# Kernel optimization log

Measured on AMD Instinct MI355X. Metric: run time of the kernel, lower is better.

The kernel has to match this reference:

```python
import jax, jax.numpy as jnp
import numpy as np

T, N, D, R, E = 512, 32, 300, 3, 64
NUM_NODES, VG = 70000, 40000


def setup_inputs() -> dict:
    key = jax.random.key(0)
    ks = jax.random.split(key, 10)
    return {
        "x_indices": jax.random.randint(ks[0], (T, N), 0, NUM_NODES),
        "edge_src": jax.random.randint(ks[1], (T, R, E), 0, N),
        "edge_dst": jax.random.randint(ks[2], (T, R, E), 0, N),
        "X": jax.random.normal(ks[3], (NUM_NODES, D), dtype=jnp.float32) * 0.1,
        "conv_W": jax.random.normal(ks[4], (R, D, D), dtype=jnp.float32) * 0.05,
        "W0": jax.random.normal(ks[5], (D, D), dtype=jnp.float32) * 0.05,
        "Wu": jax.random.normal(ks[6], (N * D, D), dtype=jnp.float32) * 0.01,
        "Uu": jax.random.normal(ks[7], (D, D), dtype=jnp.float32) * 0.05,
        "Wg": jax.random.normal(ks[8], (VG, D), dtype=jnp.float32) * 0.05,
        "bg": jnp.zeros((VG,), dtype=jnp.float32),
    }


def gcn_conv(x, W, src, dst):
    """torch_geometric GCNConv(bias=False): add self-loops, D^-1/2 (A+I) D^-1/2 (x W)."""
    n = x.shape[0]
    h = x @ W  # [N, D]
    loop = jnp.arange(n)
    s = jnp.concatenate([src, loop])
    t = jnp.concatenate([dst, loop])
    deg = jax.ops.segment_sum(jnp.ones_like(t, dtype=x.dtype), t, num_segments=n)
    dinv = jnp.where(deg > 0, jax.lax.rsqrt(jnp.maximum(deg, 1e-12)), 0.0)
    norm = dinv[s] * dinv[t]  # [E+N]
    return jax.ops.segment_sum(h[s] * norm[:, None], t, num_segments=n)


def reference(x_indices, edge_src, edge_dst, X, conv_W, W0, Wu, Uu, Wg, bg):
    def step(mem, inp):
        idx, src, dst = inp  # [N], [R,E], [R,E]
        x = X[idx]  # grapharea features [N, D]
        # sum of per-relation GCNConv outputs
        conv = jnp.sum(
            jax.vmap(gcn_conv, in_axes=(None, 0, 0, 0))(x, conv_W, src, dst), axis=0
        )
        proposed = conv + x @ W0  # eye(N) @ (x @ W0) == x @ W0
        # GRU-style update gate: [1, N*D] @ [N*D, D] + mem_row0 @ [D, D]
        gate = jax.nn.sigmoid(x.reshape(1, -1) @ Wu + mem[0:1] @ Uu)  # [1, D]
        new_mem = gate * proposed + (1.0 - gate) * mem  # broadcast over N rows
        logits = jnp.maximum(new_mem[0], 0.0) @ Wg.T + bg  # [VG]
        # memory is a non-grad buffer in torch (.data.copy_): stop gradient through time
        return jax.lax.stop_gradient(new_mem), jax.nn.log_softmax(logits)

    mem0 = jnp.zeros((N, D), dtype=X.dtype)
    _, log_probs = jax.lax.scan(step, mem0, (x_indices, edge_src, edge_dst))
    # include_senses=False: per-step torch.tensor(0) stacked -> zeros([T])
    return log_probs, jnp.zeros((x_indices.shape[0],), dtype=jnp.int32)
```

## Files before the change

### kernel.cpp

```cpp
#include <hip/hip_runtime.h>
#include <hip/hip_bf16.h>
#include <math.h>

#define T_ 512
#define N_ 32
#define D_ 300
#define R_ 3
#define E_ 64
#define VG_ 40000

typedef __attribute__((ext_vector_type(8))) short bf16x8;
typedef __attribute__((ext_vector_type(4))) float f32x4;

#define LGKM_BARRIER() asm volatile("s_waitcnt lgkmcnt(0)\n\ts_barrier" ::: "memory")

static __device__ inline unsigned short f2b(float f) {
  __hip_bfloat16 h = __float2bfloat16(f);
  return *(unsigned short*)&h;
}

__global__ void k_zero(float* __restrict__ p, int n) {
  int i = blockIdx.x * blockDim.x + threadIdx.x;
  if (i < n) p[i] = 0.f;
}

__global__ void k_tr_wu(const float* __restrict__ Wu, unsigned short* __restrict__ Wt) {
  __shared__ float s[32][33];
  int kb = blockIdx.x * 32, nb = blockIdx.y * 32;
  int tn = threadIdx.x & 31, tr = threadIdx.x >> 5;
  for (int i = tr; i < 32; i += 8) {
    int k = kb + i, n = nb + tn;
    s[i][tn] = (n < 300) ? Wu[(size_t)k * 300 + n] : 0.f;
  }
  __syncthreads();
  for (int i = tr; i < 32; i += 8) {
    int n = nb + i, k = kb + tn;
    Wt[(size_t)n * 9600 + k] = f2b(s[tn][i]);
  }
}

__global__ void k_tr_wcat(const float* __restrict__ convW, const float* __restrict__ W0,
                          unsigned short* __restrict__ Wt) {
  __shared__ float s[32][33];
  int kb = blockIdx.x * 32, nb = blockIdx.y * 32;
  int tn = threadIdx.x & 31, tr = threadIdx.x >> 5;
  for (int i = tr; i < 32; i += 8) {
    int k = kb + i, n = nb + tn;
    float v = 0.f;
    if (n < 300 && k < 1200)
      v = (k < 900) ? convW[(size_t)k * 300 + n] : W0[(size_t)(k - 900) * 300 + n];
    s[i][tn] = v;
  }
  __syncthreads();
  for (int i = tr; i < 32; i += 8) {
    int n = nb + i, k = kb + tn;
    Wt[(size_t)n * 1216 + k] = f2b(s[tn][i]);
  }
}

__global__ void k_tr_uu(const float* __restrict__ Uu, unsigned short* __restrict__ UuT) {
  __shared__ float s[32][33];
  int kb = blockIdx.x * 32, nb = blockIdx.y * 32;
  int tn = threadIdx.x & 31, tr = threadIdx.x >> 5;
  for (int i = tr; i < 32; i += 8) {
    int k = kb + i, n = nb + tn;
    s[i][tn] = (k < 300 && n < 300) ? Uu[(size_t)k * 300 + n] : 0.f;
  }
  __syncthreads();
  for (int i = tr; i < 32; i += 8) {
    int n = nb + i, k = kb + tn;
    UuT[(size_t)n * 320 + k] = f2b(s[tn][i]);
  }
}

__global__ void k_gather(const int* __restrict__ xidx, const int* __restrict__ esrc,
                         const int* __restrict__ edst, const float* __restrict__ X,
                         unsigned short* __restrict__ xg, unsigned short* __restrict__ Ag)
{
  const int t = blockIdx.x;
  __shared__ int s_idx[N_];
  __shared__ int s_src[R_][E_];
  __shared__ int s_dst[R_][E_];
  __shared__ int s_deg[R_][N_];
  __shared__ float s_dinv[R_][N_];
  const int tid = threadIdx.x;

  if (tid < N_) s_idx[tid] = xidx[t * N_ + tid];
  if (tid < R_ * E_) {
    int r = tid / E_, e = tid % E_;
    s_src[r][e] = esrc[(t * R_ + r) * E_ + e];
    s_dst[r][e] = edst[(t * R_ + r) * E_ + e];
  }
  if (tid < R_ * N_) ((int*)s_deg)[tid] = 1;
  __syncthreads();
  if (tid < R_ * E_) {
    int r = tid / E_;
    atomicAdd(&s_deg[r][s_dst[r][tid % E_]], 1);
  }
  __syncthreads();
  if (tid < R_ * N_) ((float*)s_dinv)[tid] = rsqrtf((float)((int*)s_deg)[tid]);
  __syncthreads();

  for (int nd = tid; nd < N_ * D_; nd += blockDim.x) {
    int n = nd / D_, d = nd % D_;
    xg[(size_t)t * (N_ * D_) + nd] = f2b(X[(size_t)s_idx[n] * D_ + d]);
  }
  if (tid < D_) {
    int d = tid;
    float x0 = X[(size_t)s_idx[0] * D_ + d];
    #pragma unroll
    for (int r = 0; r < R_; ++r) {
      float dinv0 = s_dinv[r][0];
      float acc = dinv0 * dinv0 * x0;
      for (int e = 0; e < E_; ++e) {
        if (s_dst[r][e] == 0) {
          int s = s_src[r][e];
          acc += s_dinv[r][s] * dinv0 * X[(size_t)s_idx[s] * D_ + d];
        }
      }
      Ag[(size_t)t * 1216 + r * D_ + d] = f2b(acc);
    }
    Ag[(size_t)t * 1216 + 900 + d] = f2b(x0);
  }
  if (tid < 16) Ag[(size_t)t * 1216 + 1200 + tid] = 0;
}

template<bool ATOMIC>
__global__ __launch_bounds__(256) void k_bgemm(
    const unsigned short* __restrict__ A,
    const unsigned short* __restrict__ B,
    float* __restrict__ C, int ldc, int Ncols, int K, int kchunk)
{
  const int tid = threadIdx.x;
  const int wid = tid >> 6, lane = tid & 63;
  const int l16 = lane & 15, lq = lane >> 4;
  const int bm = blockIdx.x * 128 + (wid & 1) * 64;
  const int bn = blockIdx.y * 128 + (wid >> 1) * 64;
  const int k0 = blockIdx.z * kchunk;
  const int nk = kchunk / 32;

  f32x4 acc[4][4] = {};
  const unsigned short* ap[4];
  const unsigned short* bp[4];
  #pragma unroll
  for (int mt = 0; mt < 4; ++mt) ap[mt] = A + (size_t)(bm + mt * 16 + l16) * K + k0 + lq * 8;
  #pragma unroll
  for (int nt = 0; nt < 4; ++nt) bp[nt] = B + (size_t)(bn + nt * 16 + l16) * K + k0 + lq * 8;

  #pragma unroll 2
  for (int c = 0; c < nk; ++c) {
    bf16x8 af[4], bfr[4];
    #pragma unroll
    for (int mt = 0; mt < 4; ++mt) af[mt] = *(const bf16x8*)(ap[mt] + c * 32);
    #pragma unroll
    for (int nt = 0; nt < 4; ++nt) bfr[nt] = *(const bf16x8*)(bp[nt] + c * 32);
    #pragma unroll
    for (int mt = 0; mt < 4; ++mt)
      #pragma unroll
      for (int nt = 0; nt < 4; ++nt)
        acc[mt][nt] = __builtin_amdgcn_mfma_f32_16x16x32_bf16(af[mt], bfr[nt], acc[mt][nt], 0, 0, 0);
  }

  #pragma unroll
  for (int mt = 0; mt < 4; ++mt) {
    #pragma unroll
    for (int r = 0; r < 4; ++r) {
      int row = bm + mt * 16 + lq * 4 + r;
      #pragma unroll
      for (int nt = 0; nt < 4; ++nt) {
        int col = bn + nt * 16 + l16;
        if (col < Ncols) {
          if (ATOMIC) atomicAdd(&C[(size_t)row * ldc + col], acc[mt][nt][r]);
          else        C[(size_t)row * ldc + col] = acc[mt][nt][r];
        }
      }
    }
  }
}

__global__ __launch_bounds__(256, 2) void k_lgemm(
    const unsigned short* __restrict__ A, const float* __restrict__ Wg,
    const float* __restrict__ bg, float* __restrict__ C)
{
  const int tid = threadIdx.x;
  const int wid = tid >> 6, lane = tid & 63;
  const int l16 = lane & 15, lq = lane >> 4;
  const int bn = blockIdx.x * 64;
  const int m0 = wid * 128;

  f32x4 acc[8][4] = {};
  const unsigned short* ap[8];
  const float* bp[4];
  #pragma unroll
  for (int mt = 0; mt < 8; ++mt) ap[mt] = A + (size_t)(m0 + mt * 16 + l16) * 320 + lq * 8;
  #pragma unroll
  for (int nt = 0; nt < 4; ++nt) bp[nt] = Wg + (size_t)(bn + nt * 16 + l16) * 300;

  #pragma unroll
  for (int c = 0; c < 10; ++c) {
    bf16x8 bfr[4];
    if (c < 9) {
      #pragma unroll
      for (int nt = 0; nt < 4; ++nt) {
        f32x4 x = *(const f32x4*)(bp[nt] + c * 32 + lq * 8);
        f32x4 y = *(const f32x4*)(bp[nt] + c * 32 + lq * 8 + 4);
        bf16x8 bv;
        #pragma unroll
        for (int j = 0; j < 4; ++j) { bv[j] = (short)f2b(x[j]); bv[4 + j] = (short)f2b(y[j]); }
        bfr[nt] = bv;
      }
    } else {
      #pragma unroll
      for (int nt = 0; nt < 4; ++nt) {
        bf16x8 bv;
        #pragma unroll
        for (int j = 0; j < 8; ++j) {
          int k = 288 + lq * 8 + j;
          bv[j] = (short)((k < 300) ? f2b(bp[nt][k]) : 0);
        }
        bfr[nt] = bv;
      }
    }
    bf16x8 af[8];
    #pragma unroll
    for (int mt = 0; mt < 8; ++mt) af[mt] = *(const bf16x8*)(ap[mt] + c * 32);
    #pragma unroll
    for (int mt = 0; mt < 8; ++mt)
      #pragma unroll
      for (int nt = 0; nt < 4; ++nt)
        acc[mt][nt] = __builtin_amdgcn_mfma_f32_16x16x32_bf16(af[mt], bfr[nt], acc[mt][nt], 0, 0, 0);
  }

  float bb[4];
  #pragma unroll
  for (int nt = 0; nt < 4; ++nt) bb[nt] = bg[bn + nt * 16 + l16];
  #pragma unroll
  for (int mt = 0; mt < 8; ++mt) {
    #pragma unroll
    for (int r = 0; r < 4; ++r) {
      int row = m0 + mt * 16 + lq * 4 + r;
      #pragma unroll
      for (int nt = 0; nt < 4; ++nt) {
        int col = bn + nt * 16 + l16;
        C[(size_t)row * VG_ + col] = acc[mt][nt][r] + bb[nt];
      }
    }
  }
}

__global__ __launch_bounds__(256, 1) void k_rec(
    const float* __restrict__ gx, const float* __restrict__ P0,
    const unsigned short* __restrict__ UuT, unsigned short* __restrict__ Mrelu_bf)
{
  __shared__ __align__(16) unsigned short m_bf[2][320];
  __shared__ unsigned short mr_s[16 * 320];
  const int tid = threadIdx.x;
  const int wid = tid >> 6, lane = tid & 63;
  const int l16 = lane & 15, lq = lane >> 4;
  const int cb = wid * 80;

  bf16x8 bfr[5][10];
  #pragma unroll
  for (int nt = 0; nt < 5; ++nt) {
    const unsigned short* bp = UuT + (size_t)(cb + nt * 16 + l16) * 320 + lq * 8;
    #pragma unroll
    for (int c = 0; c < 10; ++c)
      bfr[nt][c] = *(const bf16x8*)(bp + c * 32);
  }

  float mreg[5] = {0.f, 0.f, 0.f, 0.f, 0.f};
  float gxv[5], p0v[5];
  #pragma unroll
  for (int nt = 0; nt < 5; ++nt) {
    int c = cb + nt * 16 + l16;
    gxv[nt] = (c < 300) ? gx[c] : 0.f;
    p0v[nt] = (c < 300) ? P0[c] : 0.f;
  }

  for (int i = tid; i < 320; i += 256) { m_bf[0][i] = 0; m_bf[1][i] = 0; }
  for (int i = tid; i < 16 * 320; i += 256) mr_s[i] = 0;
  __syncthreads();

  for (int t = 0; t < T_; ++t) {
    const int rb = t & 1, wb = rb ^ 1;
    bf16x8 a[10];
    #pragma unroll
    for (int c = 0; c < 10; ++c)
      a[c] = *(const bf16x8*)(&m_bf[rb][c * 32 + lq * 8]);
    f32x4 acc0[5] = {};
    f32x4 acc1[5] = {};
    #pragma unroll
    for (int cc = 0; cc < 5; ++cc) {
      #pragma unroll
      for (int nt = 0; nt < 5; ++nt) {
        acc0[nt] = __builtin_amdgcn_mfma_f32_16x16x32_bf16(a[cc],     bfr[nt][cc],     acc0[nt], 0, 0, 0);
        acc1[nt] = __builtin_amdgcn_mfma_f32_16x16x32_bf16(a[cc + 5], bfr[nt][cc + 5], acc1[nt], 0, 0, 0);
      }
    }
    #pragma unroll
    for (int nt = 0; nt < 5; ++nt) {
      float z = acc0[nt][0] + acc1[nt][0] + gxv[nt];
      float g = __frcp_rn(1.f + __expf(-z));
      mreg[nt] = fmaf(g, p0v[nt] - mreg[nt], mreg[nt]);
    }
    const int slot = (t & 15) * 320;
    if (lq == 0) {
      #pragma unroll
      for (int nt = 0; nt < 5; ++nt) {
        int c = cb + nt * 16 + l16;
        if (c < 300) {
          m_bf[wb][c] = f2b(mreg[nt]);
          mr_s[slot + c] = f2b(fmaxf(mreg[nt], 0.f));
        }
      }
    }
    if (t + 1 < T_) {
      const size_t o = (size_t)(t + 1) * D_;
      #pragma unroll
      for (int nt = 0; nt < 5; ++nt) {
        int c = cb + nt * 16 + l16;
        if (c < 300) { gxv[nt] = gx[o + c]; p0v[nt] = P0[o + c]; }
      }
    }
    LGKM_BARRIER();
    if ((t & 7) == 7) {
      const int base = t - 7;
      const unsigned int* src = (const unsigned int*)(mr_s + (base & 15) * 320);
      unsigned int* dst = (unsigned int*)(Mrelu_bf + (size_t)base * 320);
      #pragma unroll
      for (int w = 0; w < 5; ++w) dst[tid + w * 256] = src[tid + w * 256];
    }
  }
}

__global__ __launch_bounds__(256) void k_lsm(float* __restrict__ out) {
  const int t = blockIdx.x;
  float* row = out + (size_t)t * VG_;
  const f32x4* row4 = (const f32x4*)row;
  __shared__ float redM[256];
  __shared__ float redS[256];
  const int tid = threadIdx.x;
  float lm = -1e30f, ls = 0.f;
  for (int v = tid; v < VG_ / 4; v += 256) {
    f32x4 z4 = row4[v];
    #pragma unroll
    for (int j = 0; j < 4; ++j) {
      float z = z4[j];
      float m2 = fmaxf(lm, z);
      ls = ls * expf(lm - m2) + expf(z - m2);
      lm = m2;
    }
  }
  redM[tid] = lm; redS[tid] = ls;
  __syncthreads();
  for (int s = 128; s > 0; s >>= 1) {
    if (tid < s) {
      float mA = redM[tid], mB = redM[tid + s];
      float M = fmaxf(mA, mB);
      redS[tid] = redS[tid] * expf(mA - M) + redS[tid + s] * expf(mB - M);
      redM[tid] = M;
    }
    __syncthreads();
  }
  float lse = redM[0] + logf(redS[0]);
  f32x4* row4w = (f32x4*)row;
  for (int v = tid; v < VG_ / 4; v += 256) {
    f32x4 z4 = row4w[v];
    #pragma unroll
    for (int j = 0; j < 4; ++j) z4[j] -= lse;
    row4w[v] = z4;
  }
  if (tid == 0) out[(size_t)T_ * VG_ + t] = 0.0f;
}

extern "C" void kernel_launch(void* const* d_in, const int* in_sizes, int n_in,
                              void* d_out, int out_size, void* d_ws, size_t ws_size,
                              hipStream_t stream) {
  const int*   xidx  = (const int*)d_in[0];
  const int*   esrc  = (const int*)d_in[1];
  const int*   edst  = (const int*)d_in[2];
  const float* X     = (const float*)d_in[3];
  const float* convW = (const float*)d_in[4];
  const float* W0    = (const float*)d_in[5];
  const float* Wu    = (const float*)d_in[6];
  const float* Uu    = (const float*)d_in[7];
  const float* Wg    = (const float*)d_in[8];
  const float* bg    = (const float*)d_in[9];
  float* out = (float*)d_out;

  char* ws = (char*)d_ws;
  float*          gx     = (float*)ws;
  float*          P0     = (float*)(ws + 614400);
  unsigned short* MreluB = (unsigned short*)(ws + 1228800);
  unsigned short* xgB    = (unsigned short*)(ws + 1556480);
  unsigned short* AgB    = (unsigned short*)(ws + 11386880);
  unsigned short* WuT    = (unsigned short*)(ws + 12632064);
  unsigned short* WcatT  = (unsigned short*)(ws + 20004864);
  unsigned short* UuT    = xgB;

  k_zero<<<(T_ * D_ + 255) / 256, 256, 0, stream>>>(gx, T_ * D_);
  k_tr_wu<<<dim3(300, 12), 256, 0, stream>>>(Wu, WuT);
  k_tr_wcat<<<dim3(38, 12), 256, 0, stream>>>(convW, W0, WcatT);
  k_gather<<<T_, 320, 0, stream>>>(xidx, esrc, edst, X, xgB, AgB);

  k_bgemm<true><<<dim3(4, 3, 10), 256, 0, stream>>>(xgB, WuT, gx, D_, D_, 9600, 960);
  k_bgemm<false><<<dim3(4, 3, 1), 256, 0, stream>>>(AgB, WcatT, P0, D_, D_, 1216, 1216);

  k_tr_uu<<<dim3(10, 10), 256, 0, stream>>>(Uu, UuT);
  k_rec<<<1, 256, 0, stream>>>(gx, P0, UuT, MreluB);

  k_lgemm<<<dim3(625), 256, 0, stream>>>(MreluB, Wg, bg, out);
  k_lsm<<<T_, 256, 0, stream>>>(out);
}
```

Before: 934.1 us.

## Spread recurrent kernel across 10 waves to shorten per-step MFMA chain

```diff
diff --git a/kernel.cpp b/kernel.cpp
--- a/kernel.cpp
+++ b/kernel.cpp
@@ -248,7 +248,7 @@
   }
 }
 
-__global__ __launch_bounds__(256, 1) void k_rec(
+__global__ __launch_bounds__(640, 3) void k_rec(
     const float* __restrict__ gx, const float* __restrict__ P0,
     const unsigned short* __restrict__ UuT, unsigned short* __restrict__ Mrelu_bf)
 {
@@ -257,78 +257,89 @@
   const int tid = threadIdx.x;
   const int wid = tid >> 6, lane = tid & 63;
   const int l16 = lane & 15, lq = lane >> 4;
-  const int cb = wid * 80;
-
-  bf16x8 bfr[5][10];
-  #pragma unroll
-  for (int nt = 0; nt < 5; ++nt) {
-    const unsigned short* bp = UuT + (size_t)(cb + nt * 16 + l16) * 320 + lq * 8;
+
+  const int c0 = wid * 32 + l16;
+  const int c1 = c0 + 16;
+
+  bf16x8 bfr[2][10];
+  {
+    const unsigned short* bp0 = UuT + (size_t)c0 * 320 + lq * 8;
+    const unsigned short* bp1 = UuT + (size_t)c1 * 320 + lq * 8;
+    #pragma unroll
+    for (int c = 0; c < 10; ++c) {
+      bfr[0][c] = *(const bf16x8*)(bp0 + c * 32);
+      bfr[1][c] = *(const bf16x8*)(bp1 + c * 32);
+    }
+  }
+  #pragma unroll
+  for (int nt = 0; nt < 2; ++nt)
     #pragma unroll
     for (int c = 0; c < 10; ++c)
-      bfr[nt][c] = *(const bf16x8*)(bp + c * 32);
-  }
-
-  float mreg[5] = {0.f, 0.f, 0.f, 0.f, 0.f};
-  float gxv[5], p0v[5];
-  #pragma unroll
-  for (int nt = 0; nt < 5; ++nt) {
-    int c = cb + nt * 16 + l16;
-    gxv[nt] = (c < 300) ? gx[c] : 0.f;
-    p0v[nt] = (c < 300) ? P0[c] : 0.f;
-  }
-
-  for (int i = tid; i < 320; i += 256) { m_bf[0][i] = 0; m_bf[1][i] = 0; }
-  for (int i = tid; i < 16 * 320; i += 256) mr_s[i] = 0;
+      asm("" : "+v"(bfr[nt][c]));
+
+  const int cl0 = (c0 < 299) ? c0 : 299;
+  const int cl1 = (c1 < 299) ? c1 : 299;
+  float m0 = 0.f, m1 = 0.f;
+  float gx0 = gx[cl0], gx1 = gx[cl1];
+  float p00 = P0[cl0], p01 = P0[cl1];
+
+  const f32x4 fzero = {0.f, 0.f, 0.f, 0.f};
+
+  for (int i = tid; i < 320; i += 640) { m_bf[0][i] = 0; m_bf[1][i] = 0; }
+  for (int i = tid; i < 16 * 320; i += 640) mr_s[i] = 0;
   __syncthreads();
 
   for (int t = 0; t < T_; ++t) {
     const int rb = t & 1, wb = rb ^ 1;
+    float gxn0, gxn1, p0n0, p0n1;
+    if (t + 1 < T_) {
+      const size_t o = (size_t)(t + 1) * D_;
+      gxn0 = gx[o + cl0]; gxn1 = gx[o + cl1];
+      p0n0 = P0[o + cl0]; p0n1 = P0[o + cl1];
+    }
     bf16x8 a[10];
     #pragma unroll
     for (int c = 0; c < 10; ++c)
       a[c] = *(const bf16x8*)(&m_bf[rb][c * 32 + lq * 8]);
-    f32x4 acc0[5] = {};
-    f32x4 acc1[5] = {};
-    #pragma unroll
-    for (int cc = 0; cc < 5; ++cc) {
-      #pragma unroll
-      for (int nt = 0; nt < 5; ++nt) {
-        acc0[nt] = __builtin_amdgcn_mfma_f32_16x16x32_bf16(a[cc],     bfr[nt][cc],     acc0[nt], 0, 0, 0);
-        acc1[nt] = __builtin_amdgcn_mfma_f32_16x16x32_bf16(a[cc + 5], bfr[nt][cc + 5], acc1[nt], 0, 0, 0);
-      }
-    }
-    #pragma unroll
-    for (int nt = 0; nt < 5; ++nt) {
-      float z = acc0[nt][0] + acc1[nt][0] + gxv[nt];
-      float g = __frcp_rn(1.f + __expf(-z));
-      mreg[nt] = fmaf(g, p0v[nt] - mreg[nt], mreg[nt]);
+    f32x4 A0, A1, B0, B1;
+    A0 = __builtin_amdgcn_mfma_f32_16x16x32_bf16(a[0], bfr[0][0], fzero, 0, 0, 0);
+    A1 = __builtin_amdgcn_mfma_f32_16x16x32_bf16(a[0], bfr[1][0], fzero, 0, 0, 0);
+    B0 = __builtin_amdgcn_mfma_f32_16x16x32_bf16(a[5], bfr[0][5], fzero, 0, 0, 0);
+    B1 = __builtin_amdgcn_mfma_f32_16x16x32_bf16(a[5], bfr[1][5], fzero, 0, 0, 0);
+    #pragma unroll
+    for (int cc = 1; cc < 5; ++cc) {
+      A0 = __builtin_amdgcn_mfma_f32_16x16x32_bf16(a[cc],     bfr[0][cc],     A0, 0, 0, 0);
+      A1 = __builtin_amdgcn_mfma_f32_16x16x32_bf16(a[cc],     bfr[1][cc],     A1, 0, 0, 0);
+      B0 = __builtin_amdgcn_mfma_f32_16x16x32_bf16(a[cc + 5], bfr[0][cc + 5], B0, 0, 0, 0);
+      B1 = __builtin_amdgcn_mfma_f32_16x16x32_bf16(a[cc + 5], bfr[1][cc + 5], B1, 0, 0, 0);
+    }
+    {
+      float z0 = A0[0] + B0[0] + gx0;
+      float g0 = __frcp_rn(1.f + __expf(-z0));
+      m0 = fmaf(g0, p00 - m0, m0);
+      float z1 = A1[0] + B1[0] + gx1;
+      float g1 = __frcp_rn(1.f + __expf(-z1));
+      m1 = fmaf(g1, p01 - m1, m1);
     }
     const int slot = (t & 15) * 320;
     if (lq == 0) {
-      #pragma unroll
-      for (int nt = 0; nt < 5; ++nt) {
-        int c = cb + nt * 16 + l16;
-        if (c < 300) {
-          m_bf[wb][c] = f2b(mreg[nt]);
-          mr_s[slot + c] = f2b(fmaxf(mreg[nt], 0.f));
-        }
-      }
-    }
-    if (t + 1 < T_) {
-      const size_t o = (size_t)(t + 1) * D_;
-      #pragma unroll
-      for (int nt = 0; nt < 5; ++nt) {
-        int c = cb + nt * 16 + l16;
-        if (c < 300) { gxv[nt] = gx[o + c]; p0v[nt] = P0[o + c]; }
-      }
-    }
+      if (c0 < 300) {
+        m_bf[wb][c0] = f2b(m0);
+        mr_s[slot + c0] = f2b(fmaxf(m0, 0.f));
+      }
+      if (c1 < 300) {
+        m_bf[wb][c1] = f2b(m1);
+        mr_s[slot + c1] = f2b(fmaxf(m1, 0.f));
+      }
+    }
+    gx0 = gxn0; gx1 = gxn1; p00 = p0n0; p01 = p0n1;
     LGKM_BARRIER();
     if ((t & 7) == 7) {
       const int base = t - 7;
       const unsigned int* src = (const unsigned int*)(mr_s + (base & 15) * 320);
       unsigned int* dst = (unsigned int*)(Mrelu_bf + (size_t)base * 320);
       #pragma unroll
-      for (int w = 0; w < 5; ++w) dst[tid + w * 256] = src[tid + w * 256];
+      for (int w = 0; w < 2; ++w) dst[tid + w * 640] = src[tid + w * 640];
     }
   }
 }
@@ -407,7 +418,7 @@
   k_bgemm<false><<<dim3(4, 3, 1), 256, 0, stream>>>(AgB, WcatT, P0, D_, D_, 1216, 1216);
 
   k_tr_uu<<<dim3(10, 10), 256, 0, stream>>>(Uu, UuT);
-  k_rec<<<1, 256, 0, stream>>>(gx, P0, UuT, MreluB);
+  k_rec<<<1, 640, 0, stream>>>(gx, P0, UuT, MreluB);
 
   k_lgemm<<<dim3(625), 256, 0, stream>>>(MreluB, Wg, bg, out);
   k_lsm<<<T_, 256, 0, stream>>>(out);
```

After: 811.2 us. -13.2%, faster.
